# Kernel optimization log

Hardware: AMD Instinct MI355X
Metric: run time of the kernel (lower is better)

Reference implementation:

```python
import jax, jax.numpy as jnp
import numpy as np

N_NODES = 100000
N_EDGES = 1600000
IN_DIM, FEAT_DIM, HID_DIM, OUT_DIM = 128, 64, 64, 64


def _linear_params(key, fan_in, fan_out):
    kw, kb = jax.random.split(key)
    bound = 1.0 / np.sqrt(fan_in)
    W = jax.random.uniform(kw, (fan_out, fan_in), jnp.float32, -bound, bound)
    b = jax.random.uniform(kb, (fan_out,), jnp.float32, -bound, bound)
    return W, b


def setup_inputs() -> dict:
    key = jax.random.key(0)
    k_x, k1, k2, k3, k_e = jax.random.split(key, 5)
    x = jax.random.normal(k_x, (N_NODES, IN_DIM), jnp.float32)
    edge_index = jax.random.randint(k_e, (2, N_EDGES), 0, N_NODES, jnp.int32)
    W_pre, b_pre = _linear_params(k1, IN_DIM, FEAT_DIM)
    W_first, b_first = _linear_params(k2, FEAT_DIM, HID_DIM)
    W_out, b_out = _linear_params(k3, HID_DIM, OUT_DIM)
    return {"x": x, "edge_index": edge_index,
            "W_pre": W_pre, "b_pre": b_pre,
            "W_first": W_first, "b_first": b_first,
            "W_out": W_out, "b_out": b_out}


def _gin_conv(x, src, dst, W, b):
    # out_i = nn((1+eps)*x_i + sum_{j: (j->i)} x_j), eps=0 (PyG GINConv default)
    msgs = x[src]                                   # [E, d] gather
    agg = jax.ops.segment_sum(msgs, dst, num_segments=x.shape[0])  # [N, d]
    return (x + agg) @ W.T + b


def reference(x, edge_index, W_pre, b_pre, W_first, b_first, W_out, b_out):
    src, dst = edge_index[0], edge_index[1]
    h = x @ W_pre.T + b_pre                         # feature_pre linear
    h = _gin_conv(h, src, dst, W_first, b_first)
    h = jax.nn.relu(h)                              # dropout: eval mode no-op
    h = _gin_conv(h, src, dst, W_out, b_out)
    return h
```

## Files before the change

kernel.cpp:

```cpp
#include <hip/hip_runtime.h>


using bf16x8 = __attribute__((ext_vector_type(8))) short;
using f32x4  = __attribute__((ext_vector_type(4))) float;

__device__ inline unsigned short f2bf(float f) {
    unsigned b = __float_as_uint(f);
    return (unsigned short)((b + 0x7FFF + ((b >> 16) & 1)) >> 16);
}
__device__ inline float bf2f_lo(unsigned u) { return __uint_as_float(u << 16); }
__device__ inline float bf2f_hi(unsigned u) { return __uint_as_float(u & 0xFFFF0000u); }
__device__ inline unsigned packbf(float lo, float hi) {
    return (unsigned)f2bf(lo) | ((unsigned)f2bf(hi) << 16);
}
__device__ inline void acc8(float* a, const uint4 u) {
    a[0] += bf2f_lo(u.x); a[1] += bf2f_hi(u.x);
    a[2] += bf2f_lo(u.y); a[3] += bf2f_hi(u.y);
    a[4] += bf2f_lo(u.z); a[5] += bf2f_hi(u.z);
    a[6] += bf2f_lo(u.w); a[7] += bf2f_hi(u.w);
}

constexpr int CHUNK = 8192;
constexpr int LCAP  = 2048;

__global__ __launch_bounds__(256) void k1_pre_hist(
    const float* __restrict__ x, const float* __restrict__ Wp,
    const float* __restrict__ bp, unsigned short* __restrict__ h16a, int N,
    const int* __restrict__ dst, int* __restrict__ counts,
    int E, int NBK, int NC, int GB)
{
    __shared__ char lds_raw[34816];
    const int tid = threadIdx.x;

    if (blockIdx.x >= GB) {
        int* cnt = (int*)lds_raw;
        const int c = blockIdx.x - GB;
        for (int b = tid; b < NBK; b += 256) cnt[b] = 0;
        __syncthreads();
        const int beg = c * CHUNK, end = min(beg + CHUNK, E);
        for (int e = beg + tid; e < end; e += 256)
            atomicAdd(&cnt[dst[e] >> 6], 1);
        __syncthreads();
        for (int b = tid; b < NBK; b += 256) counts[b * NC + c] = cnt[b];
        return;
    }

    constexpr int SP = 136;
    unsigned short (*xs)[SP] = (unsigned short(*)[SP])lds_raw;
    unsigned short (*ws)[SP] = (unsigned short(*)[SP])(lds_raw + 64 * SP * 2);
    const int base = blockIdx.x * 64;

    for (int i = tid; i < 64 * 32; i += 256) {
        const int r = i >> 5, q = i & 31;
        const float4 v = *(const float4*)(Wp + r * 128 + q * 4);
        *(ushort4*)&ws[r][q * 4] =
            make_ushort4(f2bf(v.x), f2bf(v.y), f2bf(v.z), f2bf(v.w));
    }
    for (int i = tid; i < 64 * 32; i += 256) {
        const int r = i >> 5, q = i & 31;
        int row = base + r; if (row > N - 1) row = N - 1;
        const float4 v = *(const float4*)(x + (size_t)row * 128 + q * 4);
        *(ushort4*)&xs[r][q * 4] =
            make_ushort4(f2bf(v.x), f2bf(v.y), f2bf(v.z), f2bf(v.w));
    }
    __syncthreads();

    const int w = tid >> 6, l = tid & 63, lr = l & 15, lg = l >> 4;
    f32x4 acc[4];
#pragma unroll
    for (int nb = 0; nb < 4; ++nb) {
        const float bv = bp[nb * 16 + lr];
        acc[nb] = (f32x4){bv, bv, bv, bv};
    }
#pragma unroll
    for (int kb = 0; kb < 4; ++kb) {
        const bf16x8 a = *(const bf16x8*)&xs[w * 16 + lr][kb * 32 + lg * 8];
#pragma unroll
        for (int nb = 0; nb < 4; ++nb) {
            const bf16x8 b = *(const bf16x8*)&ws[nb * 16 + lr][kb * 32 + lg * 8];
            acc[nb] = __builtin_amdgcn_mfma_f32_16x16x32_bf16(a, b, acc[nb], 0, 0, 0);
        }
    }
#pragma unroll
    for (int nb = 0; nb < 4; ++nb) {
#pragma unroll
        for (int r = 0; r < 4; ++r) {
            const int row = base + w * 16 + lg * 4 + r;
            if (row < N)
                h16a[(size_t)row * 64 + nb * 16 + lr] = f2bf(acc[nb][r]);
        }
    }
}

template <int RELU, int WF32>
__global__ __launch_bounds__(256) void conv_fused(
    const unsigned short* __restrict__ hin, const unsigned* __restrict__ slots,
    const int* __restrict__ counts, const float* __restrict__ W,
    const float* __restrict__ bias, float* __restrict__ outf,
    unsigned short* __restrict__ out16, int N, int E, int NC, int NBK)
{
    constexpr int SPW = 72;
    __shared__ unsigned short ws[64][SPW];
    __shared__ unsigned short xs[64][SPW];
    __shared__ unsigned lsl[LCAP];
    __shared__ int hist[64], sc[64], cur[64], loffs[65], steal;

    const int tid  = threadIdx.x;
    const int blk  = blockIdx.x;
    const int base = blk * 64;

    for (int i = tid; i < 64 * 16; i += 256) {
        const int r = i >> 4, q = i & 15;
        const float4 v = *(const float4*)(W + r * 64 + q * 4);
        *(ushort4*)&ws[r][q * 4] =
            make_ushort4(f2bf(v.x), f2bf(v.y), f2bf(v.z), f2bf(v.w));
    }

    const int beg = counts[blk * NC];
    const int end = (blk + 1 < NBK) ? counts[(blk + 1) * NC] : E;
    const int cnt  = end - beg;
    const int cntc = min(cnt, LCAP);

    if (tid < 64) hist[tid] = 0;
    if (tid == 0) steal = 0;
    __syncthreads();

    unsigned pk[8];
#pragma unroll
    for (int t = 0; t < 8; ++t) {
        const int i = tid + t * 256;
        pk[t] = (i < cntc) ? slots[beg + i] : 0xFFFFFFFFu;
    }
#pragma unroll
    for (int t = 0; t < 8; ++t)
        if (pk[t] != 0xFFFFFFFFu) atomicAdd(&hist[pk[t] >> 24], 1);
    __syncthreads();

    if (tid < 64) sc[tid] = hist[tid];
    __syncthreads();
    for (int off = 1; off < 64; off <<= 1) {
        int v = 0;
        if (tid < 64 && tid >= off) v = sc[tid - off];
        __syncthreads();
        if (tid < 64) sc[tid] += v;
        __syncthreads();
    }
    if (tid < 64) {
        const int ex = sc[tid] - hist[tid];
        loffs[tid] = ex;
        cur[tid]   = ex;
        if (tid == 63) loffs[64] = sc[63];
    }
    __syncthreads();

#pragma unroll
    for (int t = 0; t < 8; ++t)
        if (pk[t] != 0xFFFFFFFFu) {
            const int pos = atomicAdd(&cur[pk[t] >> 24], 1);
            lsl[pos] = pk[t] & 0x00FFFFFFu;
        }
    __syncthreads();

    const int l = tid & 63;
    const int leader = l & ~7;
    const int c = (l & 7) * 8;
    while (true) {
        int n = 0;
        if ((l & 7) == 0) n = atomicAdd(&steal, 1);
        n = __shfl(n, leader);
        if (n >= 64) break;
        const int node = base + n;
        float a[8] = {0.f, 0.f, 0.f, 0.f, 0.f, 0.f, 0.f, 0.f};
        if (node < N) {
            acc8(a, *(const uint4*)(hin + (size_t)node * 64 + c));
            int j = loffs[n];
            const int hi = loffs[n + 1];
            for (; j + 8 <= hi; j += 8) {
                const unsigned s0 = lsl[j],     s1 = lsl[j + 1];
                const unsigned s2 = lsl[j + 2], s3 = lsl[j + 3];
                const unsigned s4 = lsl[j + 4], s5 = lsl[j + 5];
                const unsigned s6 = lsl[j + 6], s7 = lsl[j + 7];
                const uint4 u0 = *(const uint4*)(hin + (size_t)s0 * 64 + c);
                const uint4 u1 = *(const uint4*)(hin + (size_t)s1 * 64 + c);
                const uint4 u2 = *(const uint4*)(hin + (size_t)s2 * 64 + c);
                const uint4 u3 = *(const uint4*)(hin + (size_t)s3 * 64 + c);
                const uint4 u4 = *(const uint4*)(hin + (size_t)s4 * 64 + c);
                const uint4 u5 = *(const uint4*)(hin + (size_t)s5 * 64 + c);
                const uint4 u6 = *(const uint4*)(hin + (size_t)s6 * 64 + c);
                const uint4 u7 = *(const uint4*)(hin + (size_t)s7 * 64 + c);
                acc8(a, u0); acc8(a, u1); acc8(a, u2); acc8(a, u3);
                acc8(a, u4); acc8(a, u5); acc8(a, u6); acc8(a, u7);
            }
            for (; j + 4 <= hi; j += 4) {
                const unsigned s0 = lsl[j],     s1 = lsl[j + 1];
                const unsigned s2 = lsl[j + 2], s3 = lsl[j + 3];
                const uint4 u0 = *(const uint4*)(hin + (size_t)s0 * 64 + c);
                const uint4 u1 = *(const uint4*)(hin + (size_t)s1 * 64 + c);
                const uint4 u2 = *(const uint4*)(hin + (size_t)s2 * 64 + c);
                const uint4 u3 = *(const uint4*)(hin + (size_t)s3 * 64 + c);
                acc8(a, u0); acc8(a, u1); acc8(a, u2); acc8(a, u3);
            }
            for (; j < hi; ++j)
                acc8(a, *(const uint4*)(hin + (size_t)lsl[j] * 64 + c));
            if (cnt > LCAP) {
                for (int e2 = beg + LCAP; e2 < end; ++e2) {
                    const unsigned p = slots[e2];
                    if ((int)(p >> 24) == n)
                        acc8(a, *(const uint4*)(hin + (size_t)(p & 0xFFFFFFu) * 64 + c));
                }
            }
        }
        *(uint4*)&xs[n][c] =
            make_uint4(packbf(a[0], a[1]), packbf(a[2], a[3]),
                       packbf(a[4], a[5]), packbf(a[6], a[7]));
    }
    __syncthreads();

    const int w = tid >> 6, lr = l & 15, lg = l >> 4;
    f32x4 acc[4];
#pragma unroll
    for (int nb = 0; nb < 4; ++nb) {
        const float bv = bias[nb * 16 + lr];
        acc[nb] = (f32x4){bv, bv, bv, bv};
    }
#pragma unroll
    for (int kb = 0; kb < 2; ++kb) {
        const bf16x8 a = *(const bf16x8*)&xs[w * 16 + lr][kb * 32 + lg * 8];
#pragma unroll
        for (int nb = 0; nb < 4; ++nb) {
            const bf16x8 b = *(const bf16x8*)&ws[nb * 16 + lr][kb * 32 + lg * 8];
            acc[nb] = __builtin_amdgcn_mfma_f32_16x16x32_bf16(a, b, acc[nb], 0, 0, 0);
        }
    }
#pragma unroll
    for (int nb = 0; nb < 4; ++nb) {
#pragma unroll
        for (int r = 0; r < 4; ++r) {
            const int row = base + w * 16 + lg * 4 + r;
            if (row < N) {
                float v = acc[nb][r];
                if (RELU) v = fmaxf(v, 0.f);
                if (WF32) outf[(size_t)row * 64 + nb * 16 + lr] = v;
                else      out16[(size_t)row * 64 + nb * 16 + lr] = f2bf(v);
            }
        }
    }
}

__global__ __launch_bounds__(512) void k_blocksum(
    const int* __restrict__ in, int* __restrict__ partial, int n)
{
    __shared__ int s[512];
    const int i = blockIdx.x * 512 + threadIdx.x;
    s[threadIdx.x] = (i < n) ? in[i] : 0;
    __syncthreads();
    for (int off = 256; off > 0; off >>= 1) {
        if (threadIdx.x < off) s[threadIdx.x] += s[threadIdx.x + off];
        __syncthreads();
    }
    if (threadIdx.x == 0) partial[blockIdx.x] = s[0];
}

__global__ __launch_bounds__(1024) void k_scanpartial1024(
    int* __restrict__ partial, int nblk)
{
    __shared__ int s[1024];
    const int t = threadIdx.x;
    s[t] = (t < nblk) ? partial[t] : 0;
    __syncthreads();
    for (int off = 1; off < 1024; off <<= 1) {
        const int v = (t >= off) ? s[t - off] : 0;
        __syncthreads();
        s[t] += v;
        __syncthreads();
    }
    if (t < nblk) partial[t] = (t == 0) ? 0 : s[t - 1];
}

__global__ __launch_bounds__(512) void k_exscan(
    int* __restrict__ data, const int* __restrict__ partial, int n)
{
    __shared__ int s[512];
    const int i = blockIdx.x * 512 + threadIdx.x;
    const int t = threadIdx.x;
    const int v = (i < n) ? data[i] : 0;
    s[t] = v;
    __syncthreads();
    for (int off = 1; off < 512; off <<= 1) {
        const int u = (t >= off) ? s[t - off] : 0;
        __syncthreads();
        s[t] += u;
        __syncthreads();
    }
    if (i < n) data[i] = partial[blockIdx.x] + s[t] - v;
}

__global__ __launch_bounds__(256) void p_scatter(
    const int* __restrict__ src, const int* __restrict__ dst,
    const int* __restrict__ counts, unsigned* __restrict__ slots,
    int E, int NBK, int NC)
{
    __shared__ int cur[1600];
    const int c = blockIdx.x;
    for (int b = threadIdx.x; b < NBK; b += 256) cur[b] = counts[b * NC + c];
    __syncthreads();
    const int beg = c * CHUNK;
    const int end = min(beg + CHUNK, E);
    for (int e = beg + threadIdx.x; e < end; e += 256) {
        const int d = dst[e];
        const int pos = atomicAdd(&cur[d >> 6], 1);
        slots[pos] = ((unsigned)(d & 63) << 24) | (unsigned)src[e];
    }
}

extern "C" void kernel_launch(void* const* d_in, const int* in_sizes, int n_in,
                              void* d_out, int out_size, void* d_ws, size_t ws_size,
                              hipStream_t stream)
{
    const float* x       = (const float*)d_in[0];
    const int*   ei      = (const int*)  d_in[1];
    const float* W_pre   = (const float*)d_in[2];
    const float* b_pre   = (const float*)d_in[3];
    const float* W_first = (const float*)d_in[4];
    const float* b_first = (const float*)d_in[5];
    const float* W_out   = (const float*)d_in[6];
    const float* b_out   = (const float*)d_in[7];

    const int N = in_sizes[0] / 128;
    const int E = in_sizes[1] / 2;
    const int* src = ei;
    const int* dst = ei + E;

    const int NBK   = (N + 63) / 64;
    const int NC    = (E + CHUNK - 1) / CHUNK;
    const int nscan = NBK * NC;
    const int nsblk = (nscan + 511) / 512;

    unsigned short* h16a   = (unsigned short*)d_ws;
    unsigned short* h16b   = h16a + (size_t)N * 64;
    unsigned*       slots  = (unsigned*)(h16b + (size_t)N * 64);
    int*            counts = (int*)(slots + E);
    int*            partial= counts + nscan;

    float* out = (float*)d_out;
    const int GB = (N + 63) / 64;

    k1_pre_hist<<<GB + NC, 256, 0, stream>>>(
        x, W_pre, b_pre, h16a, N, dst, counts, E, NBK, NC, GB);

    k_blocksum<<<nsblk, 512, 0, stream>>>(counts, partial, nscan);
    k_scanpartial1024<<<1, 1024, 0, stream>>>(partial, nsblk);
    k_exscan<<<nsblk, 512, 0, stream>>>(counts, partial, nscan);

    p_scatter<<<NC, 256, 0, stream>>>(src, dst, counts, slots, E, NBK, NC);

    conv_fused<1, 0><<<NBK, 256, 0, stream>>>(
        h16a, slots, counts, W_first, b_first, nullptr, h16b, N, E, NC, NBK);

    conv_fused<0, 1><<<NBK, 256, 0, stream>>>(
        h16b, slots, counts, W_out, b_out, out, nullptr, N, E, NC, NBK);
}
```

Before: 137.2 us.

## Build full CSR via two-level radix partition instead of per-block local sort

Replaces the single-pass 64-node bucket scatter with a coarse 512-node bucket scatter followed by a per-bucket fine sort kernel that produces a true CSR (per-node offsets and sorted source list). The conv kernels no longer run a local histogram, scan and scatter each time, which removes that work from both convolution passes. The chunk size is halved so the coarse scatter runs with more blocks. In exchange there is an extra kernel launch and a second full pass over the edge slots, plus extra workspace for slots2 and noffs.

New measurement: 140.4 us. 2.3% more time.

```diff
diff --git a/kernel.cpp b/kernel.cpp
--- a/kernel.cpp
+++ b/kernel.cpp
@@ -20,14 +20,14 @@
     a[6] += bf2f_lo(u.w); a[7] += bf2f_hi(u.w);
 }
 
-constexpr int CHUNK = 8192;
+constexpr int CHUNK = 4096;
 constexpr int LCAP  = 2048;
 
 __global__ __launch_bounds__(256) void k1_pre_hist(
     const float* __restrict__ x, const float* __restrict__ Wp,
     const float* __restrict__ bp, unsigned short* __restrict__ h16a, int N,
-    const int* __restrict__ dst, int* __restrict__ counts,
-    int E, int NBK, int NC, int GB)
+    const int* __restrict__ dst, int* __restrict__ ccounts,
+    int E, int NBKC, int NC, int GB)
 {
     __shared__ char lds_raw[34816];
     const int tid = threadIdx.x;
@@ -35,13 +35,13 @@
     if (blockIdx.x >= GB) {
         int* cnt = (int*)lds_raw;
         const int c = blockIdx.x - GB;
-        for (int b = tid; b < NBK; b += 256) cnt[b] = 0;
+        for (int b = tid; b < NBKC; b += 256) cnt[b] = 0;
         __syncthreads();
         const int beg = c * CHUNK, end = min(beg + CHUNK, E);
         for (int e = beg + tid; e < end; e += 256)
-            atomicAdd(&cnt[dst[e] >> 6], 1);
-        __syncthreads();
-        for (int b = tid; b < NBK; b += 256) counts[b * NC + c] = cnt[b];
+            atomicAdd(&cnt[dst[e] >> 9], 1);
+        __syncthreads();
+        for (int b = tid; b < NBKC; b += 256) ccounts[b * NC + c] = cnt[b];
         return;
     }
 
@@ -92,22 +92,135 @@
     }
 }
 
+__global__ __launch_bounds__(512) void k_blocksum(
+    const int* __restrict__ in, int* __restrict__ partial, int n)
+{
+    __shared__ int s[512];
+    const int i = blockIdx.x * 512 + threadIdx.x;
+    s[threadIdx.x] = (i < n) ? in[i] : 0;
+    __syncthreads();
+    for (int off = 256; off > 0; off >>= 1) {
+        if (threadIdx.x < off) s[threadIdx.x] += s[threadIdx.x + off];
+        __syncthreads();
+    }
+    if (threadIdx.x == 0) partial[blockIdx.x] = s[0];
+}
+
+__global__ __launch_bounds__(1024) void k_scanpartial1024(
+    int* __restrict__ partial, int nblk)
+{
+    __shared__ int s[1024];
+    const int t = threadIdx.x;
+    s[t] = (t < nblk) ? partial[t] : 0;
+    __syncthreads();
+    for (int off = 1; off < 1024; off <<= 1) {
+        const int v = (t >= off) ? s[t - off] : 0;
+        __syncthreads();
+        s[t] += v;
+        __syncthreads();
+    }
+    if (t < nblk) partial[t] = (t == 0) ? 0 : s[t - 1];
+}
+
+__global__ __launch_bounds__(512) void k_exscan(
+    int* __restrict__ data, const int* __restrict__ partial, int n)
+{
+    __shared__ int s[512];
+    const int i = blockIdx.x * 512 + threadIdx.x;
+    const int t = threadIdx.x;
+    const int v = (i < n) ? data[i] : 0;
+    s[t] = v;
+    __syncthreads();
+    for (int off = 1; off < 512; off <<= 1) {
+        const int u = (t >= off) ? s[t - off] : 0;
+        __syncthreads();
+        s[t] += u;
+        __syncthreads();
+    }
+    if (i < n) data[i] = partial[blockIdx.x] + s[t] - v;
+}
+
+__global__ __launch_bounds__(256) void p_coarse(
+    const int* __restrict__ src, const int* __restrict__ dst,
+    const int* __restrict__ ccounts, unsigned* __restrict__ slots,
+    int E, int NBKC, int NC)
+{
+    __shared__ int cur[256];
+    const int c = blockIdx.x;
+    for (int b = threadIdx.x; b < NBKC; b += 256) cur[b] = ccounts[b * NC + c];
+    __syncthreads();
+    const int beg = c * CHUNK;
+    const int end = min(beg + CHUNK, E);
+    for (int e = beg + threadIdx.x; e < end; e += 256) {
+        const int d = dst[e];
+        const int pos = atomicAdd(&cur[d >> 9], 1);
+        slots[pos] = ((unsigned)(d & 511) << 23) | (unsigned)src[e];
+    }
+}
+
+__global__ __launch_bounds__(256) void p_fine(
+    const unsigned* __restrict__ slots, const int* __restrict__ ccounts,
+    unsigned* __restrict__ slots2, int* __restrict__ noffs,
+    int E, int N, int NBKC, int NC)
+{
+    __shared__ int hist[512], psum[256], start[512], cur[512];
+    const int cb  = blockIdx.x;
+    const int tid = threadIdx.x;
+    const int cbase = ccounts[cb * NC];
+    const int cend  = (cb + 1 < NBKC) ? ccounts[(cb + 1) * NC] : E;
+
+    hist[tid] = 0; hist[tid + 256] = 0;
+    __syncthreads();
+    for (int i = cbase + tid; i < cend; i += 256)
+        atomicAdd(&hist[slots[i] >> 23], 1);
+    __syncthreads();
+
+    const int pair = hist[2 * tid] + hist[2 * tid + 1];
+    psum[tid] = pair;
+    __syncthreads();
+    for (int off = 1; off < 256; off <<= 1) {
+        const int v = (tid >= off) ? psum[tid - off] : 0;
+        __syncthreads();
+        psum[tid] += v;
+        __syncthreads();
+    }
+    const int ex = psum[tid] - pair;
+    start[2 * tid]     = ex;
+    start[2 * tid + 1] = ex + hist[2 * tid];
+    __syncthreads();
+
+    for (int l9 = tid; l9 < 512; l9 += 256) {
+        const int o = cbase + start[l9];
+        cur[l9] = o;
+        const int gnode = cb * 512 + l9;
+        if (gnode < N) noffs[gnode] = o;
+    }
+    if (cb == NBKC - 1 && tid == 0) noffs[N] = cend;
+    __syncthreads();
+
+    for (int i = cbase + tid; i < cend; i += 256) {
+        const unsigned p = slots[i];
+        const int pos = atomicAdd(&cur[p >> 23], 1);
+        slots2[pos] = p & 0x7FFFFFu;
+    }
+}
+
 template <int RELU, int WF32>
 __global__ __launch_bounds__(256) void conv_fused(
-    const unsigned short* __restrict__ hin, const unsigned* __restrict__ slots,
-    const int* __restrict__ counts, const float* __restrict__ W,
+    const unsigned short* __restrict__ hin, const unsigned* __restrict__ slots2,
+    const int* __restrict__ noffs, const float* __restrict__ W,
     const float* __restrict__ bias, float* __restrict__ outf,
-    unsigned short* __restrict__ out16, int N, int E, int NC, int NBK)
+    unsigned short* __restrict__ out16, int N)
 {
     constexpr int SPW = 72;
     __shared__ unsigned short ws[64][SPW];
     __shared__ unsigned short xs[64][SPW];
     __shared__ unsigned lsl[LCAP];
-    __shared__ int hist[64], sc[64], cur[64], loffs[65], steal;
+    __shared__ int loffs[65];
+    __shared__ int steal;
 
     const int tid  = threadIdx.x;
-    const int blk  = blockIdx.x;
-    const int base = blk * 64;
+    const int base = blockIdx.x * 64;
 
     for (int i = tid; i < 64 * 16; i += 256) {
         const int r = i >> 4, q = i & 15;
@@ -115,50 +228,13 @@
         *(ushort4*)&ws[r][q * 4] =
             make_ushort4(f2bf(v.x), f2bf(v.y), f2bf(v.z), f2bf(v.w));
     }
-
-    const int beg = counts[blk * NC];
-    const int end = (blk + 1 < NBK) ? counts[(blk + 1) * NC] : E;
-    const int cnt  = end - beg;
-    const int cntc = min(cnt, LCAP);
-
-    if (tid < 64) hist[tid] = 0;
+    if (tid <= 64) loffs[tid] = noffs[min(base + tid, N)];
     if (tid == 0) steal = 0;
     __syncthreads();
 
-    unsigned pk[8];
-#pragma unroll
-    for (int t = 0; t < 8; ++t) {
-        const int i = tid + t * 256;
-        pk[t] = (i < cntc) ? slots[beg + i] : 0xFFFFFFFFu;
-    }
-#pragma unroll
-    for (int t = 0; t < 8; ++t)
-        if (pk[t] != 0xFFFFFFFFu) atomicAdd(&hist[pk[t] >> 24], 1);
-    __syncthreads();
-
-    if (tid < 64) sc[tid] = hist[tid];
-    __syncthreads();
-    for (int off = 1; off < 64; off <<= 1) {
-        int v = 0;
-        if (tid < 64 && tid >= off) v = sc[tid - off];
-        __syncthreads();
-        if (tid < 64) sc[tid] += v;
-        __syncthreads();
-    }
-    if (tid < 64) {
-        const int ex = sc[tid] - hist[tid];
-        loffs[tid] = ex;
-        cur[tid]   = ex;
-        if (tid == 63) loffs[64] = sc[63];
-    }
-    __syncthreads();
-
-#pragma unroll
-    for (int t = 0; t < 8; ++t)
-        if (pk[t] != 0xFFFFFFFFu) {
-            const int pos = atomicAdd(&cur[pk[t] >> 24], 1);
-            lsl[pos] = pk[t] & 0x00FFFFFFu;
-        }
+    const int beg = loffs[0];
+    const int cnt = loffs[64] - beg;
+    for (int i = tid; i < min(cnt, LCAP); i += 256) lsl[i] = slots2[beg + i];
     __syncthreads();
 
     const int l = tid & 63;
@@ -173,9 +249,10 @@
         float a[8] = {0.f, 0.f, 0.f, 0.f, 0.f, 0.f, 0.f, 0.f};
         if (node < N) {
             acc8(a, *(const uint4*)(hin + (size_t)node * 64 + c));
-            int j = loffs[n];
-            const int hi = loffs[n + 1];
-            for (; j + 8 <= hi; j += 8) {
+            int j = loffs[n] - beg;
+            const int hi = loffs[n + 1] - beg;
+            const int hiL = min(hi, LCAP);
+            for (; j + 8 <= hiL; j += 8) {
                 const unsigned s0 = lsl[j],     s1 = lsl[j + 1];
                 const unsigned s2 = lsl[j + 2], s3 = lsl[j + 3];
                 const unsigned s4 = lsl[j + 4], s5 = lsl[j + 5];
@@ -191,7 +268,7 @@
                 acc8(a, u0); acc8(a, u1); acc8(a, u2); acc8(a, u3);
                 acc8(a, u4); acc8(a, u5); acc8(a, u6); acc8(a, u7);
             }
-            for (; j + 4 <= hi; j += 4) {
+            for (; j + 4 <= hiL; j += 4) {
                 const unsigned s0 = lsl[j],     s1 = lsl[j + 1];
                 const unsigned s2 = lsl[j + 2], s3 = lsl[j + 3];
                 const uint4 u0 = *(const uint4*)(hin + (size_t)s0 * 64 + c);
@@ -200,14 +277,11 @@
                 const uint4 u3 = *(const uint4*)(hin + (size_t)s3 * 64 + c);
                 acc8(a, u0); acc8(a, u1); acc8(a, u2); acc8(a, u3);
             }
-            for (; j < hi; ++j)
+            for (; j < hiL; ++j)
                 acc8(a, *(const uint4*)(hin + (size_t)lsl[j] * 64 + c));
-            if (cnt > LCAP) {
-                for (int e2 = beg + LCAP; e2 < end; ++e2) {
-                    const unsigned p = slots[e2];
-                    if ((int)(p >> 24) == n)
-                        acc8(a, *(const uint4*)(hin + (size_t)(p & 0xFFFFFFu) * 64 + c));
-                }
+            for (; j < hi; ++j) {
+                const unsigned s = slots2[beg + j];
+                acc8(a, *(const uint4*)(hin + (size_t)s * 64 + c));
             }
         }
         *(uint4*)&xs[n][c] =
@@ -247,72 +321,6 @@
     }
 }
 
-__global__ __launch_bounds__(512) void k_blocksum(
-    const int* __restrict__ in, int* __restrict__ partial, int n)
-{
-    __shared__ int s[512];
-    const int i = blockIdx.x * 512 + threadIdx.x;
-    s[threadIdx.x] = (i < n) ? in[i] : 0;
-    __syncthreads();
-    for (int off = 256; off > 0; off >>= 1) {
-        if (threadIdx.x < off) s[threadIdx.x] += s[threadIdx.x + off];
-        __syncthreads();
-    }
-    if (threadIdx.x == 0) partial[blockIdx.x] = s[0];
-}
-
-__global__ __launch_bounds__(1024) void k_scanpartial1024(
-    int* __restrict__ partial, int nblk)
-{
-    __shared__ int s[1024];
-    const int t = threadIdx.x;
-    s[t] = (t < nblk) ? partial[t] : 0;
-    __syncthreads();
-    for (int off = 1; off < 1024; off <<= 1) {
-        const int v = (t >= off) ? s[t - off] : 0;
-        __syncthreads();
-        s[t] += v;
-        __syncthreads();
-    }
-    if (t < nblk) partial[t] = (t == 0) ? 0 : s[t - 1];
-}
-
-__global__ __launch_bounds__(512) void k_exscan(
-    int* __restrict__ data, const int* __restrict__ partial, int n)
-{
-    __shared__ int s[512];
-    const int i = blockIdx.x * 512 + threadIdx.x;
-    const int t = threadIdx.x;
-    const int v = (i < n) ? data[i] : 0;
-    s[t] = v;
-    __syncthreads();
-    for (int off = 1; off < 512; off <<= 1) {
-        const int u = (t >= off) ? s[t - off] : 0;
-        __syncthreads();
-        s[t] += u;
-        __syncthreads();
-    }
-    if (i < n) data[i] = partial[blockIdx.x] + s[t] - v;
-}
-
-__global__ __launch_bounds__(256) void p_scatter(
-    const int* __restrict__ src, const int* __restrict__ dst,
-    const int* __restrict__ counts, unsigned* __restrict__ slots,
-    int E, int NBK, int NC)
-{
-    __shared__ int cur[1600];
-    const int c = blockIdx.x;
-    for (int b = threadIdx.x; b < NBK; b += 256) cur[b] = counts[b * NC + c];
-    __syncthreads();
-    const int beg = c * CHUNK;
-    const int end = min(beg + CHUNK, E);
-    for (int e = beg + threadIdx.x; e < end; e += 256) {
-        const int d = dst[e];
-        const int pos = atomicAdd(&cur[d >> 6], 1);
-        slots[pos] = ((unsigned)(d & 63) << 24) | (unsigned)src[e];
-    }
-}
-
 extern "C" void kernel_launch(void* const* d_in, const int* in_sizes, int n_in,
                               void* d_out, int out_size, void* d_ws, size_t ws_size,
                               hipStream_t stream)
@@ -331,32 +339,35 @@
     const int* src = ei;
     const int* dst = ei + E;
 
-    const int NBK   = (N + 63) / 64;
+    const int NBKC  = (N + 511) / 512;
     const int NC    = (E + CHUNK - 1) / CHUNK;
-    const int nscan = NBK * NC;
+    const int nscan = NBKC * NC;
     const int nsblk = (nscan + 511) / 512;
+    const int GB    = (N + 63) / 64;
 
     unsigned short* h16a   = (unsigned short*)d_ws;
     unsigned short* h16b   = h16a + (size_t)N * 64;
     unsigned*       slots  = (unsigned*)(h16b + (size_t)N * 64);
-    int*            counts = (int*)(slots + E);
-    int*            partial= counts + nscan;
+    unsigned*       slots2 = slots + E;
+    int*            ccounts= (int*)(slots2 + E);
+    int*            partial= ccounts + nscan;
+    int*            noffs  = partial + 1024;
 
     float* out = (float*)d_out;
-    const int GB = (N + 63) / 64;
 
     k1_pre_hist<<<GB + NC, 256, 0, stream>>>(
-        x, W_pre, b_pre, h16a, N, dst, counts, E, NBK, NC, GB);
-
-    k_blocksum<<<nsblk, 512, 0, stream>>>(counts, partial, nscan);
+        x, W_pre, b_pre, h16a, N, dst, ccounts, E, NBKC, NC, GB);
+
+    k_blocksum<<<nsblk, 512, 0, stream>>>(ccounts, partial, nscan);
     k_scanpartial1024<<<1, 1024, 0, stream>>>(partial, nsblk);
-    k_exscan<<<nsblk, 512, 0, stream>>>(counts, partial, nscan);
-
-    p_scatter<<<NC, 256, 0, stream>>>(src, dst, counts, slots, E, NBK, NC);
-
-    conv_fused<1, 0><<<NBK, 256, 0, stream>>>(
-        h16a, slots, counts, W_first, b_first, nullptr, h16b, N, E, NC, NBK);
-
-    conv_fused<0, 1><<<NBK, 256, 0, stream>>>(
-        h16b, slots, counts, W_out, b_out, out, nullptr, N, E, NC, NBK);
-}
+    k_exscan<<<nsblk, 512, 0, stream>>>(ccounts, partial, nscan);
+
+    p_coarse<<<NC, 256, 0, stream>>>(src, dst, ccounts, slots, E, NBKC, NC);
+    p_fine<<<NBKC, 256, 0, stream>>>(slots, ccounts, slots2, noffs, E, N, NBKC, NC);
+
+    conv_fused<1, 0><<<GB, 256, 0, stream>>>(
+        h16a, slots2, noffs, W_first, b_first, nullptr, h16b, N);
+
+    conv_fused<0, 1><<<GB, 256, 0, stream>>>(
+        h16b, slots2, noffs, W_out, b_out, out, nullptr, N);
+}
```
